# Performance work log

Measured on AMD Instinct MI355X. Metric: run time of the kernel, lower is better.

The kernel has to match this reference:

```python
import jax, jax.numpy as jnp
import numpy as np

NUM_HEADS = 16
ROPE_BASE = 2048.0


def _rope_tables(seq_len, head_dim, dtype):
    inv_freq = 1.0 / (ROPE_BASE ** (jnp.arange(0, head_dim, 2, dtype=jnp.float32) / head_dim))
    t = jnp.arange(seq_len, dtype=jnp.float32)
    freqs = jnp.einsum('i,j->ij', t, inv_freq)          # [N, D/2]
    emb = jnp.concatenate([freqs, freqs], axis=-1)       # [N, D]
    return jnp.cos(emb).astype(dtype), jnp.sin(emb).astype(dtype)


def _rotate_half(x):
    x1, x2 = jnp.split(x, 2, axis=-1)
    return jnp.concatenate([-x2, x1], axis=-1)


def setup_inputs() -> dict:
    key = jax.random.key(0)
    k1, k2, k3, k4 = jax.random.split(key, 4)
    B, N, C = 2, 2048, 1024
    x = jax.random.normal(k1, (B, N, C), dtype=jnp.float32)
    w_qkv = jax.random.normal(k2, (3 * C, C), dtype=jnp.float32) * (C ** -0.5)
    w_proj = jax.random.normal(k3, (C, C), dtype=jnp.float32) * (C ** -0.5)
    b_proj = jnp.zeros((C,), dtype=jnp.float32)
    key_padding_mask = jax.random.randint(k4, (B, N), 0, 2, dtype=jnp.int32)
    return {"x": x, "w_qkv": w_qkv, "w_proj": w_proj, "b_proj": b_proj,
            "key_padding_mask": key_padding_mask}


def reference(x, w_qkv, w_proj, b_proj, key_padding_mask):
    B, N, C = x.shape
    H = NUM_HEADS
    D = C // H
    scale = D ** -0.5

    qkv = x @ w_qkv.T                                    # [B, N, 3C]
    q, k, v = jnp.split(qkv, 3, axis=-1)
    # [B, N, C] -> [B, H, N, D]
    q = q.reshape(B, N, H, D).transpose(0, 2, 1, 3)
    k = k.reshape(B, N, H, D).transpose(0, 2, 1, 3)
    v = v.reshape(B, N, H, D).transpose(0, 2, 1, 3)

    cos, sin = _rope_tables(N, D, x.dtype)               # [N, D]
    q = q * cos + _rotate_half(q) * sin
    k = k * cos + _rotate_half(k) * sin

    attn = jnp.einsum('bhqd,bhkd->bhqk', q, k) * scale   # [B, H, N, N]
    mask = (key_padding_mask == 0)[:, None, None, :]     # [B, 1, 1, N]
    attn = jnp.where(mask, jnp.asarray(-1e9, attn.dtype), attn)
    attn = jax.nn.softmax(attn, axis=-1)

    out = jnp.einsum('bhqk,bhkd->bhqd', attn, v)         # [B, H, N, D]
    out = out.transpose(0, 2, 1, 3).reshape(B, N, C)
    return out @ w_proj.T + b_proj
```

## Files before the change

kernel.cpp:

```cpp
#include <hip/hip_runtime.h>


typedef __attribute__((ext_vector_type(8))) short          s16x8;
typedef __attribute__((ext_vector_type(8))) unsigned short u16x8;
typedef __attribute__((ext_vector_type(4))) unsigned short u16x4;
typedef __attribute__((ext_vector_type(4))) float          f32x4;

#define MFMA_BF16(a, b, c) __builtin_amdgcn_mfma_f32_16x16x32_bf16((a), (b), (c), 0, 0, 0)

#define GLD_TO_LDS(gp, lp) __builtin_amdgcn_global_load_lds(                  \
    (const __attribute__((address_space(1))) void*)(gp),                      \
    (__attribute__((address_space(3))) void*)(lp), 16, 0, 0)

__device__ __forceinline__ unsigned short f2bf(float f) {
    union { float f; unsigned int u; } v; v.f = f;
    unsigned int u = v.u;
    unsigned int r = u + 0x7FFFu + ((u >> 16) & 1u);
    return (unsigned short)(r >> 16);
}
__device__ __forceinline__ float bf2f(unsigned short h) {
    union { unsigned int u; float f; } v; v.u = ((unsigned int)h) << 16;
    return v.f;
}

__global__ __launch_bounds__(256) void prep(const float* __restrict__ x,
                                            const float* __restrict__ wqkv,
                                            const float* __restrict__ wproj,
                                            const int* __restrict__ m,
                                            unsigned short* __restrict__ xb,
                                            unsigned short* __restrict__ wqkvb,
                                            unsigned short* __restrict__ wprojb,
                                            unsigned short* __restrict__ mb) {
    int blk = blockIdx.x, tid = threadIdx.x;
    if (blk < 8192) {
        const float* src; unsigned short* dst; int i;
        if (blk < 4096)      { src = x;     dst = xb;     i = blk * 256 + tid; }
        else if (blk < 7168) { src = wqkv;  dst = wqkvb;  i = (blk - 4096) * 256 + tid; }
        else                 { src = wproj; dst = wprojb; i = (blk - 7168) * 256 + tid; }
        f32x4 v = ((const f32x4*)src)[i];
        u16x4 o;
        o[0] = f2bf(v[0]); o[1] = f2bf(v[1]); o[2] = f2bf(v[2]); o[3] = f2bf(v[3]);
        ((u16x4*)dst)[i] = o;
    } else {
        int i = (blk - 8192) * 256 + tid;
        mb[i] = (m[i] == 0) ? (unsigned short)0 : (unsigned short)0x3F80;
    }
}

__global__ __launch_bounds__(256) void gemm_bt(const unsigned short* __restrict__ A,
                                               const unsigned short* __restrict__ B,
                                               unsigned short* __restrict__ C,
                                               int M, int N, int K) {
    __shared__ unsigned short Al[128][64];
    __shared__ unsigned short Bl[128][64];
    const int tid  = threadIdx.x;
    const int lane = tid & 63;
    const int qd   = lane >> 4;
    const int cc   = lane & 15;
    const int wave = tid >> 6;
    const int wr   = wave >> 1, wc = wave & 1;
    const int m0   = blockIdx.y * 128, n0 = blockIdx.x * 128;
    unsigned short* Alf = &Al[0][0];
    unsigned short* Blf = &Bl[0][0];

    f32x4 acc[4][4];
#pragma unroll
    for (int i = 0; i < 4; i++)
#pragma unroll
        for (int j = 0; j < 4; j++) acc[i][j] = (f32x4){0.f, 0.f, 0.f, 0.f};

    for (int k0 = 0; k0 < K; k0 += 64) {
#pragma unroll
        for (int t = 0; t < 4; t++) {
            int idx = t * 256 + tid;
            int row = idx >> 3, sg = (idx & 7) ^ (row & 7);
            GLD_TO_LDS(A + (size_t)(m0 + row) * K + k0 + sg * 8, Alf + idx * 8);
            GLD_TO_LDS(B + (size_t)(n0 + row) * K + k0 + sg * 8, Blf + idx * 8);
        }
        __syncthreads();
#pragma unroll
        for (int ks = 0; ks < 64; ks += 32) {
            const int s4 = ks >> 3;
            s16x8 af[4], bf[4];
#pragma unroll
            for (int i = 0; i < 4; i++) {
                int r = wr * 64 + i * 16 + cc;
                af[i] = *(const s16x8*)&Al[r][((s4 + qd) ^ (r & 7)) * 8];
            }
#pragma unroll
            for (int j = 0; j < 4; j++) {
                int r = wc * 64 + j * 16 + cc;
                bf[j] = *(const s16x8*)&Bl[r][((s4 + qd) ^ (r & 7)) * 8];
            }
#pragma unroll
            for (int i = 0; i < 4; i++)
#pragma unroll
                for (int j = 0; j < 4; j++)
                    acc[i][j] = MFMA_BF16(af[i], bf[j], acc[i][j]);
        }
        __syncthreads();
    }
#pragma unroll
    for (int i = 0; i < 4; i++)
#pragma unroll
        for (int j = 0; j < 4; j++)
#pragma unroll
            for (int r = 0; r < 4; r++) {
                int row = m0 + wr * 64 + i * 16 + qd * 4 + r;
                int col = n0 + wc * 64 + j * 16 + cc;
                C[(size_t)row * N + col] = f2bf(acc[i][j][r]);
            }
}

__global__ __launch_bounds__(256) void rope_scatter(const unsigned short* __restrict__ qkv,
                                                    const int* __restrict__ msk,
                                                    unsigned short* __restrict__ Q,
                                                    unsigned short* __restrict__ Kg,
                                                    unsigned short* __restrict__ Vt) {
    const int N = 2048, H = 16, D = 64, C3 = 3072;
    const float SCL = 0.18033688f;
    __shared__ unsigned short vl[64][65];
    const int nt = blockIdx.x, h = blockIdx.y, b = blockIdx.z;
    const int n0 = nt * 64;
    const int tid = threadIdx.x;
    const size_t bh = (size_t)b * H + h;
#pragma unroll
    for (int it = 0; it < 2; it++) {
        int idx = tid + it * 256;
        int row = idx >> 3, seg = idx & 7;
        int d0 = seg * 8;
        int n = n0 + row;
        size_t rb = ((size_t)b * N + n) * C3;
        int keep = msk[(size_t)b * N + n];
        u16x8 qv = *(const u16x8*)&qkv[rb + h * 64 + d0];
        u16x8 qp = *(const u16x8*)&qkv[rb + h * 64 + (d0 ^ 32)];
        u16x8 kv = *(const u16x8*)&qkv[rb + 1024 + h * 64 + d0];
        u16x8 kp = *(const u16x8*)&qkv[rb + 1024 + h * 64 + (d0 ^ 32)];
        u16x8 vv = *(const u16x8*)&qkv[rb + 2048 + h * 64 + d0];
        u16x8 qo, ko;
        float sgn = (d0 < 32) ? -1.0f : 1.0f;
#pragma unroll
        for (int j = 0; j < 8; j++) {
            int jj = (d0 & 31) + j;
            float th = (float)n * exp2f(-0.34375f * (float)jj);
            float cth = cosf(th), sth = sinf(th);
            qo[j] = f2bf((bf2f(qv[j]) * cth + sgn * bf2f(qp[j]) * sth) * SCL);
            ko[j] = f2bf(bf2f(kv[j]) * cth + sgn * bf2f(kp[j]) * sth);
            vl[row][d0 + j] = keep ? vv[j] : (unsigned short)0;
        }
        *(u16x8*)&Q[(bh * N + n) * D + d0]  = qo;
        *(u16x8*)&Kg[(bh * N + n) * D + d0] = ko;
    }
    __syncthreads();
#pragma unroll
    for (int it = 0; it < 2; it++) {
        int idx = tid + it * 256;
        int drow = idx >> 3, nseg = idx & 7;
        u16x8 ov;
#pragma unroll
        for (int j = 0; j < 8; j++) ov[j] = vl[nseg * 8 + j][drow];
        *(u16x8*)&Vt[(bh * D + drow) * N + n0 + nseg * 8] = ov;
    }
}

__global__ __launch_bounds__(256, 2) void flash_attn(const unsigned short* __restrict__ Q,
                                                     const unsigned short* __restrict__ Kg,
                                                     const unsigned short* __restrict__ Vt,
                                                     const unsigned short* __restrict__ mb,
                                                     unsigned short* __restrict__ Og) {
    const int N = 2048, H = 16, D = 64;
    __shared__ unsigned short Kl0[64][64], Kl1[64][64];
    __shared__ unsigned short Vl0[64][64], Vl1[64][64];
    __shared__ unsigned short Pl[4][32][76];
    const int tid  = threadIdx.x;
    const int lane = tid & 63;
    const int wave = tid >> 6;
    const int qd   = lane >> 4;
    const int cc   = lane & 15;
    const int qt = blockIdx.x, h = blockIdx.y, b = blockIdx.z;
    const int q0 = qt * 128;
    const size_t bh = (size_t)b * H + h;

    s16x8 qf[2][2];
#pragma unroll
    for (int fr = 0; fr < 2; fr++) {
        const unsigned short* Qb = Q + (bh * N + q0 + wave * 32 + fr * 16 + cc) * D;
        qf[fr][0] = *(const s16x8*)(Qb + qd * 8);
        qf[fr][1] = *(const s16x8*)(Qb + 32 + qd * 8);
    }

    f32x4 o[2][4], lacc[2];
#pragma unroll
    for (int fr = 0; fr < 2; fr++) {
        lacc[fr] = (f32x4){0.f, 0.f, 0.f, 0.f};
#pragma unroll
        for (int db = 0; db < 4; db++) o[fr][db] = (f32x4){0.f, 0.f, 0.f, 0.f};
    }

    const unsigned short* Kbase = Kg + bh * N * D;
    const unsigned short* Vbase = Vt + bh * D * N;
    const unsigned short* mbase = mb + (size_t)b * N;
    const int row_s = tid >> 3, sg_s = (tid & 7) ^ ((tid >> 3) & 7);
    const int row_s2 = (tid + 256) >> 3, sg_s2 = (tid & 7) ^ (((tid + 256) >> 3) & 7);

    auto issue = [&](int k0, unsigned short* Kb, unsigned short* Vb) {
        GLD_TO_LDS(Kbase + (size_t)(k0 + row_s) * D + sg_s * 8,  Kb + tid * 8);
        GLD_TO_LDS(Vbase + (size_t)row_s * N + k0 + sg_s * 8,    Vb + tid * 8);
        GLD_TO_LDS(Kbase + (size_t)(k0 + row_s2) * D + sg_s2 * 8, Kb + (tid + 256) * 8);
        GLD_TO_LDS(Vbase + (size_t)row_s2 * N + k0 + sg_s2 * 8,   Vb + (tid + 256) * 8);
    };

    auto compute = [&](int k0, const unsigned short (*Kb)[64], const unsigned short (*Vb)[64]) {
        f32x4 sst[4][2];
        __builtin_amdgcn_s_setprio(1);
#pragma unroll
        for (int sub = 0; sub < 4; sub++) {
            int kr = sub * 16 + cc;
            s16x8 kf0 = *(const s16x8*)&Kb[kr][((0 + qd) ^ (kr & 7)) * 8];
            s16x8 kf1 = *(const s16x8*)&Kb[kr][((4 + qd) ^ (kr & 7)) * 8];
#pragma unroll
            for (int fr = 0; fr < 2; fr++) {
                f32x4 s = (f32x4){0.f, 0.f, 0.f, 0.f};
                s = MFMA_BF16(kf0, qf[fr][0], s);
                sst[sub][fr] = MFMA_BF16(kf1, qf[fr][1], s);
            }
        }
        __builtin_amdgcn_s_setprio(0);

        auto sm = [&](int sub) {
#pragma unroll
            for (int fr = 0; fr < 2; fr++) {
                f32x4 s = sst[sub][fr];
                float p0 = exp2f(s[0]);
                float p1 = exp2f(s[1]);
                float p2 = exp2f(s[2]);
                float p3 = exp2f(s[3]);
                unsigned int w0 = __builtin_amdgcn_perm(
                    __builtin_bit_cast(unsigned int, p1),
                    __builtin_bit_cast(unsigned int, p0), 0x07060302u);
                unsigned int w1 = __builtin_amdgcn_perm(
                    __builtin_bit_cast(unsigned int, p3),
                    __builtin_bit_cast(unsigned int, p2), 0x07060302u);
                unsigned long long w = ((unsigned long long)w1 << 32) | w0;
                *(unsigned long long*)&Pl[wave][fr * 16 + cc][sub * 16 + qd * 4] = w;
            }
        };

        auto pv = [&](int ks) {
            s16x8 mf = *(const s16x8*)&mbase[k0 + ks * 32 + qd * 8];
            s16x8 vfl[4];
#pragma unroll
            for (int db = 0; db < 4; db++) {
                int vr = db * 16 + cc;
                vfl[db] = *(const s16x8*)&Vb[vr][((ks * 4 + qd) ^ (vr & 7)) * 8];
            }
            __builtin_amdgcn_s_setprio(1);
#pragma unroll
            for (int fr = 0; fr < 2; fr++) {
                s16x8 pf = *(const s16x8*)&Pl[wave][fr * 16 + cc][ks * 32 + qd * 8];
                lacc[fr] = MFMA_BF16(pf, mf, lacc[fr]);
#pragma unroll
                for (int db = 0; db < 4; db++)
                    o[fr][db] = MFMA_BF16(pf, vfl[db], o[fr][db]);
            }
            __builtin_amdgcn_s_setprio(0);
        };

        sm(0); sm(1);
        pv(0);
        sm(2); sm(3);
        pv(1);
    };

    issue(0, &Kl0[0][0], &Vl0[0][0]);
    __syncthreads();
    for (int it = 0; it < 32; it += 2) {
        int k0 = it * 64;
        if (it + 1 < 32) issue(k0 + 64, &Kl1[0][0], &Vl1[0][0]);
        compute(k0, Kl0, Vl0);
        __syncthreads();
        if (it + 2 < 32) issue(k0 + 128, &Kl0[0][0], &Vl0[0][0]);
        compute(k0 + 64, Kl1, Vl1);
        __syncthreads();
    }

#pragma unroll
    for (int fr = 0; fr < 2; fr++) {
        float linv[4];
#pragma unroll
        for (int r = 0; r < 4; r++) linv[r] = 1.0f / lacc[fr][r];
#pragma unroll
        for (int db = 0; db < 4; db++)
#pragma unroll
            for (int r = 0; r < 4; r++) {
                int n = q0 + wave * 32 + fr * 16 + qd * 4 + r;
                Og[((size_t)b * N + n) * 1024 + h * 64 + db * 16 + cc] =
                    f2bf(o[fr][db][r] * linv[r]);
            }
    }
}

__global__ __launch_bounds__(256) void gemm_proj(const unsigned short* __restrict__ A,
                                                 const unsigned short* __restrict__ B,
                                                 float* __restrict__ C,
                                                 const float* __restrict__ bias) {
    const int NN = 1024, K = 1024;
    __shared__ unsigned short Al[128][64];
    __shared__ unsigned short Bl[64][64];
    const int tid  = threadIdx.x;
    const int lane = tid & 63;
    const int qd   = lane >> 4;
    const int cc   = lane & 15;
    const int wave = tid >> 6;
    const int wr   = wave >> 1, wc = wave & 1;
    const int m0   = blockIdx.y * 128, n0 = blockIdx.x * 64;
    unsigned short* Alf = &Al[0][0];
    unsigned short* Blf = &Bl[0][0];

    f32x4 acc[4][2];
#pragma unroll
    for (int i = 0; i < 4; i++)
#pragma unroll
        for (int j = 0; j < 2; j++) acc[i][j] = (f32x4){0.f, 0.f, 0.f, 0.f};

    for (int k0 = 0; k0 < K; k0 += 64) {
#pragma unroll
        for (int t = 0; t < 4; t++) {
            int idx = t * 256 + tid;
            int row = idx >> 3, sg = (idx & 7) ^ (row & 7);
            GLD_TO_LDS(A + (size_t)(m0 + row) * K + k0 + sg * 8, Alf + idx * 8);
        }
#pragma unroll
        for (int t = 0; t < 2; t++) {
            int idx = t * 256 + tid;
            int row = idx >> 3, sg = (idx & 7) ^ (row & 7);
            GLD_TO_LDS(B + (size_t)(n0 + row) * K + k0 + sg * 8, Blf + idx * 8);
        }
        __syncthreads();
#pragma unroll
        for (int ks = 0; ks < 64; ks += 32) {
            const int s4 = ks >> 3;
            s16x8 af[4], bf[2];
#pragma unroll
            for (int i = 0; i < 4; i++) {
                int r = wr * 64 + i * 16 + cc;
                af[i] = *(const s16x8*)&Al[r][((s4 + qd) ^ (r & 7)) * 8];
            }
#pragma unroll
            for (int j = 0; j < 2; j++) {
                int r = wc * 32 + j * 16 + cc;
                bf[j] = *(const s16x8*)&Bl[r][((s4 + qd) ^ (r & 7)) * 8];
            }
#pragma unroll
            for (int i = 0; i < 4; i++)
#pragma unroll
                for (int j = 0; j < 2; j++)
                    acc[i][j] = MFMA_BF16(af[i], bf[j], acc[i][j]);
        }
        __syncthreads();
    }
#pragma unroll
    for (int i = 0; i < 4; i++)
#pragma unroll
        for (int j = 0; j < 2; j++)
#pragma unroll
            for (int r = 0; r < 4; r++) {
                int row = m0 + wr * 64 + i * 16 + qd * 4 + r;
                int col = n0 + wc * 32 + j * 16 + cc;
                C[(size_t)row * NN + col] = acc[i][j][r] + bias[col];
            }
}

extern "C" void kernel_launch(void* const* d_in, const int* in_sizes, int n_in,
                              void* d_out, int out_size, void* d_ws, size_t ws_size,
                              hipStream_t stream) {
    const float* x      = (const float*)d_in[0];
    const float* w_qkv  = (const float*)d_in[1];
    const float* w_proj = (const float*)d_in[2];
    const float* b_proj = (const float*)d_in[3];
    const int*   mask   = (const int*)d_in[4];
    float* out = (float*)d_out;

    unsigned short* ws     = (unsigned short*)d_ws;
    unsigned short* xb     = ws;
    unsigned short* wqkvb  = xb     + (size_t)4096 * 1024;
    unsigned short* wprojb = wqkvb  + (size_t)3072 * 1024;
    unsigned short* qkv    = wprojb + (size_t)1024 * 1024;
    unsigned short* Qm     = qkv    + (size_t)4096 * 3072;
    unsigned short* Km     = Qm     + (size_t)32 * 2048 * 64;
    unsigned short* Vtm    = Km     + (size_t)32 * 2048 * 64;
    unsigned short* attno  = Vtm    + (size_t)32 * 2048 * 64;
    unsigned short* maskbf = attno  + (size_t)4096 * 1024;

    prep<<<8208, 256, 0, stream>>>(x, w_qkv, w_proj, mask, xb, wqkvb, wprojb, maskbf);
    gemm_bt<<<dim3(24, 32), 256, 0, stream>>>(xb, wqkvb, qkv, 4096, 3072, 1024);
    rope_scatter<<<dim3(32, 16, 2), 256, 0, stream>>>(qkv, mask, Qm, Km, Vtm);
    flash_attn<<<dim3(16, 16, 2), 256, 0, stream>>>(Qm, Km, Vtm, maskbf, attno);
    gemm_proj<<<dim3(16, 32), 256, 0, stream>>>(attno, wprojb, out, b_proj);
}
```

Before: 200.1 us.

## Split flash attention block into eight waves of sixteen query rows each

Doubles the flash attention block to 512 threads with each wave owning 16 query rows instead of 32. This halves per-wave accumulator registers and the per-thread K/V staging loads, aiming for more resident waves and better latency hiding. In exchange each K/V fragment read from LDS feeds only one query fragment, doubling LDS read traffic per MFMA. The mask fragment loads are hoisted to the start of each tile.

Result: no change. 199.4 us (-0.4%).

```diff
diff --git a/kernel.cpp b/kernel.cpp
--- a/kernel.cpp
+++ b/kernel.cpp
@@ -163,7 +163,7 @@
     }
 }
 
-__global__ __launch_bounds__(256, 2) void flash_attn(const unsigned short* __restrict__ Q,
+__global__ __launch_bounds__(512, 4) void flash_attn(const unsigned short* __restrict__ Q,
                                                      const unsigned short* __restrict__ Kg,
                                                      const unsigned short* __restrict__ Vt,
                                                      const unsigned short* __restrict__ mb,
@@ -171,7 +171,7 @@
     const int N = 2048, H = 16, D = 64;
     __shared__ unsigned short Kl0[64][64], Kl1[64][64];
     __shared__ unsigned short Vl0[64][64], Vl1[64][64];
-    __shared__ unsigned short Pl[4][32][76];
+    __shared__ unsigned short Pl[8][16][76];
     const int tid  = threadIdx.x;
     const int lane = tid & 63;
     const int wave = tid >> 6;
@@ -181,95 +181,80 @@
     const int q0 = qt * 128;
     const size_t bh = (size_t)b * H + h;
 
-    s16x8 qf[2][2];
-#pragma unroll
-    for (int fr = 0; fr < 2; fr++) {
-        const unsigned short* Qb = Q + (bh * N + q0 + wave * 32 + fr * 16 + cc) * D;
-        qf[fr][0] = *(const s16x8*)(Qb + qd * 8);
-        qf[fr][1] = *(const s16x8*)(Qb + 32 + qd * 8);
-    }
-
-    f32x4 o[2][4], lacc[2];
-#pragma unroll
-    for (int fr = 0; fr < 2; fr++) {
-        lacc[fr] = (f32x4){0.f, 0.f, 0.f, 0.f};
-#pragma unroll
-        for (int db = 0; db < 4; db++) o[fr][db] = (f32x4){0.f, 0.f, 0.f, 0.f};
-    }
+    s16x8 qf[2];
+    {
+        const unsigned short* Qb = Q + (bh * N + q0 + wave * 16 + cc) * D;
+        qf[0] = *(const s16x8*)(Qb + qd * 8);
+        qf[1] = *(const s16x8*)(Qb + 32 + qd * 8);
+    }
+
+    f32x4 o[4], lacc = (f32x4){0.f, 0.f, 0.f, 0.f};
+#pragma unroll
+    for (int db = 0; db < 4; db++) o[db] = (f32x4){0.f, 0.f, 0.f, 0.f};
 
     const unsigned short* Kbase = Kg + bh * N * D;
     const unsigned short* Vbase = Vt + bh * D * N;
     const unsigned short* mbase = mb + (size_t)b * N;
     const int row_s = tid >> 3, sg_s = (tid & 7) ^ ((tid >> 3) & 7);
-    const int row_s2 = (tid + 256) >> 3, sg_s2 = (tid & 7) ^ (((tid + 256) >> 3) & 7);
 
     auto issue = [&](int k0, unsigned short* Kb, unsigned short* Vb) {
-        GLD_TO_LDS(Kbase + (size_t)(k0 + row_s) * D + sg_s * 8,  Kb + tid * 8);
-        GLD_TO_LDS(Vbase + (size_t)row_s * N + k0 + sg_s * 8,    Vb + tid * 8);
-        GLD_TO_LDS(Kbase + (size_t)(k0 + row_s2) * D + sg_s2 * 8, Kb + (tid + 256) * 8);
-        GLD_TO_LDS(Vbase + (size_t)row_s2 * N + k0 + sg_s2 * 8,   Vb + (tid + 256) * 8);
+        GLD_TO_LDS(Kbase + (size_t)(k0 + row_s) * D + sg_s * 8, Kb + tid * 8);
+        GLD_TO_LDS(Vbase + (size_t)row_s * N + k0 + sg_s * 8,   Vb + tid * 8);
     };
 
     auto compute = [&](int k0, const unsigned short (*Kb)[64], const unsigned short (*Vb)[64]) {
-        f32x4 sst[4][2];
+        s16x8 mf0 = *(const s16x8*)&mbase[k0 + qd * 8];
+        s16x8 mf1 = *(const s16x8*)&mbase[k0 + 32 + qd * 8];
+
+        f32x4 sst[4];
         __builtin_amdgcn_s_setprio(1);
 #pragma unroll
         for (int sub = 0; sub < 4; sub++) {
             int kr = sub * 16 + cc;
             s16x8 kf0 = *(const s16x8*)&Kb[kr][((0 + qd) ^ (kr & 7)) * 8];
             s16x8 kf1 = *(const s16x8*)&Kb[kr][((4 + qd) ^ (kr & 7)) * 8];
-#pragma unroll
-            for (int fr = 0; fr < 2; fr++) {
-                f32x4 s = (f32x4){0.f, 0.f, 0.f, 0.f};
-                s = MFMA_BF16(kf0, qf[fr][0], s);
-                sst[sub][fr] = MFMA_BF16(kf1, qf[fr][1], s);
-            }
+            f32x4 s = (f32x4){0.f, 0.f, 0.f, 0.f};
+            s = MFMA_BF16(kf0, qf[0], s);
+            sst[sub] = MFMA_BF16(kf1, qf[1], s);
         }
         __builtin_amdgcn_s_setprio(0);
 
         auto sm = [&](int sub) {
-#pragma unroll
-            for (int fr = 0; fr < 2; fr++) {
-                f32x4 s = sst[sub][fr];
-                float p0 = exp2f(s[0]);
-                float p1 = exp2f(s[1]);
-                float p2 = exp2f(s[2]);
-                float p3 = exp2f(s[3]);
-                unsigned int w0 = __builtin_amdgcn_perm(
-                    __builtin_bit_cast(unsigned int, p1),
-                    __builtin_bit_cast(unsigned int, p0), 0x07060302u);
-                unsigned int w1 = __builtin_amdgcn_perm(
-                    __builtin_bit_cast(unsigned int, p3),
-                    __builtin_bit_cast(unsigned int, p2), 0x07060302u);
-                unsigned long long w = ((unsigned long long)w1 << 32) | w0;
-                *(unsigned long long*)&Pl[wave][fr * 16 + cc][sub * 16 + qd * 4] = w;
-            }
+            f32x4 s = sst[sub];
+            float p0 = exp2f(s[0]);
+            float p1 = exp2f(s[1]);
+            float p2 = exp2f(s[2]);
+            float p3 = exp2f(s[3]);
+            unsigned int w0 = __builtin_amdgcn_perm(
+                __builtin_bit_cast(unsigned int, p1),
+                __builtin_bit_cast(unsigned int, p0), 0x07060302u);
+            unsigned int w1 = __builtin_amdgcn_perm(
+                __builtin_bit_cast(unsigned int, p3),
+                __builtin_bit_cast(unsigned int, p2), 0x07060302u);
+            unsigned long long w = ((unsigned long long)w1 << 32) | w0;
+            *(unsigned long long*)&Pl[wave][cc][sub * 16 + qd * 4] = w;
         };
 
-        auto pv = [&](int ks) {
-            s16x8 mf = *(const s16x8*)&mbase[k0 + ks * 32 + qd * 8];
+        auto pv = [&](int ks, s16x8 mf) {
             s16x8 vfl[4];
 #pragma unroll
             for (int db = 0; db < 4; db++) {
                 int vr = db * 16 + cc;
                 vfl[db] = *(const s16x8*)&Vb[vr][((ks * 4 + qd) ^ (vr & 7)) * 8];
             }
+            s16x8 pf = *(const s16x8*)&Pl[wave][cc][ks * 32 + qd * 8];
             __builtin_amdgcn_s_setprio(1);
-#pragma unroll
-            for (int fr = 0; fr < 2; fr++) {
-                s16x8 pf = *(const s16x8*)&Pl[wave][fr * 16 + cc][ks * 32 + qd * 8];
-                lacc[fr] = MFMA_BF16(pf, mf, lacc[fr]);
-#pragma unroll
-                for (int db = 0; db < 4; db++)
-                    o[fr][db] = MFMA_BF16(pf, vfl[db], o[fr][db]);
-            }
+            lacc = MFMA_BF16(pf, mf, lacc);
+#pragma unroll
+            for (int db = 0; db < 4; db++)
+                o[db] = MFMA_BF16(pf, vfl[db], o[db]);
             __builtin_amdgcn_s_setprio(0);
         };
 
         sm(0); sm(1);
-        pv(0);
+        pv(0, mf0);
         sm(2); sm(3);
-        pv(1);
+        pv(1, mf1);
     };
 
     issue(0, &Kl0[0][0], &Vl0[0][0]);
@@ -284,20 +269,17 @@
         __syncthreads();
     }
 
-#pragma unroll
-    for (int fr = 0; fr < 2; fr++) {
-        float linv[4];
-#pragma unroll
-        for (int r = 0; r < 4; r++) linv[r] = 1.0f / lacc[fr][r];
-#pragma unroll
-        for (int db = 0; db < 4; db++)
-#pragma unroll
-            for (int r = 0; r < 4; r++) {
-                int n = q0 + wave * 32 + fr * 16 + qd * 4 + r;
-                Og[((size_t)b * N + n) * 1024 + h * 64 + db * 16 + cc] =
-                    f2bf(o[fr][db][r] * linv[r]);
-            }
-    }
+    float linv[4];
+#pragma unroll
+    for (int r = 0; r < 4; r++) linv[r] = 1.0f / lacc[r];
+#pragma unroll
+    for (int db = 0; db < 4; db++)
+#pragma unroll
+        for (int r = 0; r < 4; r++) {
+            int n = q0 + wave * 16 + qd * 4 + r;
+            Og[((size_t)b * N + n) * 1024 + h * 64 + db * 16 + cc] =
+                f2bf(o[db][r] * linv[r]);
+        }
 }
 
 __global__ __launch_bounds__(256) void gemm_proj(const unsigned short* __restrict__ A,
@@ -395,6 +377,6 @@
     prep<<<8208, 256, 0, stream>>>(x, w_qkv, w_proj, mask, xb, wqkvb, wprojb, maskbf);
     gemm_bt<<<dim3(24, 32), 256, 0, stream>>>(xb, wqkvb, qkv, 4096, 3072, 1024);
     rope_scatter<<<dim3(32, 16, 2), 256, 0, stream>>>(qkv, mask, Qm, Km, Vtm);
-    flash_attn<<<dim3(16, 16, 2), 256, 0, stream>>>(Qm, Km, Vtm, maskbf, attno);
+    flash_attn<<<dim3(16, 16, 2), 512, 0, stream>>>(Qm, Km, Vtm, maskbf, attno);
     gemm_proj<<<dim3(16, 32), 256, 0, stream>>>(attno, wprojb, out, b_proj);
 }
```

## Switch flash attention to 32x32 MFMA with register-resident P and permuted V/mask layout

Applied to the files above, without the earlier changes.

Moves the flash-attention kernel from 16x16x32 to 32x32x16 bf16 MFMAs. The QK^T output accumulator is fed straight into the PV MFMA as the A operand, which removes the per-wave LDS staging buffer for P. To make that register reuse valid, the prep and V-transpose kernels now permute key positions within each group of 16 so the mask and V^T columns line up with the 32x32 accumulator row ordering. This cuts LDS traffic and instruction count but relies on the permutation being exactly right and raises per-lane accumulator register use.

Measured after the change: 189.4 us. 1.06x faster.

```diff
diff --git a/kernel.cpp b/kernel.cpp
--- a/kernel.cpp
+++ b/kernel.cpp
@@ -5,8 +5,11 @@
 typedef __attribute__((ext_vector_type(8))) unsigned short u16x8;
 typedef __attribute__((ext_vector_type(4))) unsigned short u16x4;
 typedef __attribute__((ext_vector_type(4))) float          f32x4;
+typedef __attribute__((ext_vector_type(16))) float         f32x16;
+typedef __attribute__((ext_vector_type(4))) unsigned int   u32x4;
 
 #define MFMA_BF16(a, b, c) __builtin_amdgcn_mfma_f32_16x16x32_bf16((a), (b), (c), 0, 0, 0)
+#define MFMA32_BF16(a, b, c) __builtin_amdgcn_mfma_f32_32x32x16_bf16((a), (b), (c), 0, 0, 0)
 
 #define GLD_TO_LDS(gp, lp) __builtin_amdgcn_global_load_lds(                  \
     (const __attribute__((address_space(1))) void*)(gp),                      \
@@ -21,6 +24,19 @@
 __device__ __forceinline__ float bf2f(unsigned short h) {
     union { unsigned int u; float f; } v; v.u = ((unsigned int)h) << 16;
     return v.f;
+}
+__device__ __forceinline__ f32x16 zero16() {
+    f32x16 z;
+#pragma unroll
+    for (int i = 0; i < 16; i++) z[i] = 0.f;
+    return z;
+}
+__device__ __forceinline__ unsigned int pkbf(float a, float b) {
+    return __builtin_amdgcn_perm(__builtin_bit_cast(unsigned int, b),
+                                 __builtin_bit_cast(unsigned int, a), 0x07060302u);
+}
+__device__ __forceinline__ int perm16(int p) {
+    return (p & 3) + 8 * ((p >> 2) & 1) + 4 * (p >> 3);
 }
 
 __global__ __launch_bounds__(256) void prep(const float* __restrict__ x,
@@ -43,7 +59,8 @@
         ((u16x4*)dst)[i] = o;
     } else {
         int i = (blk - 8192) * 256 + tid;
-        mb[i] = (m[i] == 0) ? (unsigned short)0 : (unsigned short)0x3F80;
+        int src = (i & ~15) | perm16(i & 15);
+        mb[i] = (m[src] == 0) ? (unsigned short)0 : (unsigned short)0x3F80;
     }
 }
 
@@ -158,7 +175,11 @@
         int drow = idx >> 3, nseg = idx & 7;
         u16x8 ov;
 #pragma unroll
-        for (int j = 0; j < 8; j++) ov[j] = vl[nseg * 8 + j][drow];
+        for (int j = 0; j < 8; j++) {
+            int cpos = nseg * 8 + j;
+            int srcl = (cpos & ~15) | perm16(cpos & 15);
+            ov[j] = vl[srcl][drow];
+        }
         *(u16x8*)&Vt[(bh * D + drow) * N + n0 + nseg * 8] = ov;
     }
 }
@@ -171,31 +192,24 @@
     const int N = 2048, H = 16, D = 64;
     __shared__ unsigned short Kl0[64][64], Kl1[64][64];
     __shared__ unsigned short Vl0[64][64], Vl1[64][64];
-    __shared__ unsigned short Pl[4][32][76];
     const int tid  = threadIdx.x;
     const int lane = tid & 63;
     const int wave = tid >> 6;
-    const int qd   = lane >> 4;
-    const int cc   = lane & 15;
+    const int c    = lane & 31;
+    const int hi   = lane >> 5;
     const int qt = blockIdx.x, h = blockIdx.y, b = blockIdx.z;
     const int q0 = qt * 128;
     const size_t bh = (size_t)b * H + h;
 
-    s16x8 qf[2][2];
-#pragma unroll
-    for (int fr = 0; fr < 2; fr++) {
-        const unsigned short* Qb = Q + (bh * N + q0 + wave * 32 + fr * 16 + cc) * D;
-        qf[fr][0] = *(const s16x8*)(Qb + qd * 8);
-        qf[fr][1] = *(const s16x8*)(Qb + 32 + qd * 8);
-    }
-
-    f32x4 o[2][4], lacc[2];
-#pragma unroll
-    for (int fr = 0; fr < 2; fr++) {
-        lacc[fr] = (f32x4){0.f, 0.f, 0.f, 0.f};
-#pragma unroll
-        for (int db = 0; db < 4; db++) o[fr][db] = (f32x4){0.f, 0.f, 0.f, 0.f};
-    }
+    s16x8 qf[4];
+    {
+        const unsigned short* Qb = Q + (bh * N + q0 + wave * 32 + c) * D;
+#pragma unroll
+        for (int kd = 0; kd < 4; kd++) qf[kd] = *(const s16x8*)(Qb + kd * 16 + hi * 8);
+    }
+
+    f32x16 o[2], lacc;
+    o[0] = zero16(); o[1] = zero16(); lacc = zero16();
 
     const unsigned short* Kbase = Kg + bh * N * D;
     const unsigned short* Vbase = Vt + bh * D * N;
@@ -204,72 +218,61 @@
     const int row_s2 = (tid + 256) >> 3, sg_s2 = (tid & 7) ^ (((tid + 256) >> 3) & 7);
 
     auto issue = [&](int k0, unsigned short* Kb, unsigned short* Vb) {
-        GLD_TO_LDS(Kbase + (size_t)(k0 + row_s) * D + sg_s * 8,  Kb + tid * 8);
-        GLD_TO_LDS(Vbase + (size_t)row_s * N + k0 + sg_s * 8,    Vb + tid * 8);
+        GLD_TO_LDS(Kbase + (size_t)(k0 + row_s) * D + sg_s * 8,   Kb + tid * 8);
+        GLD_TO_LDS(Vbase + (size_t)row_s * N + k0 + sg_s * 8,     Vb + tid * 8);
         GLD_TO_LDS(Kbase + (size_t)(k0 + row_s2) * D + sg_s2 * 8, Kb + (tid + 256) * 8);
         GLD_TO_LDS(Vbase + (size_t)row_s2 * N + k0 + sg_s2 * 8,   Vb + (tid + 256) * 8);
     };
 
     auto compute = [&](int k0, const unsigned short (*Kb)[64], const unsigned short (*Vb)[64]) {
-        f32x4 sst[4][2];
+        f32x16 sst[2];
         __builtin_amdgcn_s_setprio(1);
 #pragma unroll
-        for (int sub = 0; sub < 4; sub++) {
-            int kr = sub * 16 + cc;
-            s16x8 kf0 = *(const s16x8*)&Kb[kr][((0 + qd) ^ (kr & 7)) * 8];
-            s16x8 kf1 = *(const s16x8*)&Kb[kr][((4 + qd) ^ (kr & 7)) * 8];
-#pragma unroll
-            for (int fr = 0; fr < 2; fr++) {
-                f32x4 s = (f32x4){0.f, 0.f, 0.f, 0.f};
-                s = MFMA_BF16(kf0, qf[fr][0], s);
-                sst[sub][fr] = MFMA_BF16(kf1, qf[fr][1], s);
-            }
+        for (int kg = 0; kg < 2; kg++) {
+            int kr = kg * 32 + c;
+            f32x16 s = zero16();
+#pragma unroll
+            for (int kd = 0; kd < 4; kd++) {
+                s16x8 kf = *(const s16x8*)&Kb[kr][((kd * 2 + hi) ^ (kr & 7)) * 8];
+                s = MFMA32_BF16(kf, qf[kd], s);
+            }
+            sst[kg] = s;
         }
         __builtin_amdgcn_s_setprio(0);
 
-        auto sm = [&](int sub) {
-#pragma unroll
-            for (int fr = 0; fr < 2; fr++) {
-                f32x4 s = sst[sub][fr];
-                float p0 = exp2f(s[0]);
-                float p1 = exp2f(s[1]);
-                float p2 = exp2f(s[2]);
-                float p3 = exp2f(s[3]);
-                unsigned int w0 = __builtin_amdgcn_perm(
-                    __builtin_bit_cast(unsigned int, p1),
-                    __builtin_bit_cast(unsigned int, p0), 0x07060302u);
-                unsigned int w1 = __builtin_amdgcn_perm(
-                    __builtin_bit_cast(unsigned int, p3),
-                    __builtin_bit_cast(unsigned int, p2), 0x07060302u);
-                unsigned long long w = ((unsigned long long)w1 << 32) | w0;
-                *(unsigned long long*)&Pl[wave][fr * 16 + cc][sub * 16 + qd * 4] = w;
+        auto packkg = [&](int kg, s16x8* pa) {
+            float p[16];
+#pragma unroll
+            for (int r = 0; r < 16; r++) p[r] = __builtin_amdgcn_exp2f(sst[kg][r]);
+#pragma unroll
+            for (int half = 0; half < 2; half++) {
+                int bs = half * 8;
+                u32x4 w = { pkbf(p[bs + 0], p[bs + 1]), pkbf(p[bs + 2], p[bs + 3]),
+                            pkbf(p[bs + 4], p[bs + 5]), pkbf(p[bs + 6], p[bs + 7]) };
+                pa[half] = __builtin_bit_cast(s16x8, w);
             }
         };
 
-        auto pv = [&](int ks) {
-            s16x8 mf = *(const s16x8*)&mbase[k0 + ks * 32 + qd * 8];
-            s16x8 vfl[4];
-#pragma unroll
-            for (int db = 0; db < 4; db++) {
-                int vr = db * 16 + cc;
-                vfl[db] = *(const s16x8*)&Vb[vr][((ks * 4 + qd) ^ (vr & 7)) * 8];
-            }
+        auto pvks = [&](int ks, s16x8 pf) {
+            s16x8 mfr = *(const s16x8*)&mbase[k0 + ks * 16 + hi * 8];
             __builtin_amdgcn_s_setprio(1);
-#pragma unroll
-            for (int fr = 0; fr < 2; fr++) {
-                s16x8 pf = *(const s16x8*)&Pl[wave][fr * 16 + cc][ks * 32 + qd * 8];
-                lacc[fr] = MFMA_BF16(pf, mf, lacc[fr]);
-#pragma unroll
-                for (int db = 0; db < 4; db++)
-                    o[fr][db] = MFMA_BF16(pf, vfl[db], o[fr][db]);
+            lacc = MFMA32_BF16(pf, mfr, lacc);
+#pragma unroll
+            for (int db = 0; db < 2; db++) {
+                int vr = db * 32 + c;
+                s16x8 vf = *(const s16x8*)&Vb[vr][((ks * 2 + hi) ^ (vr & 7)) * 8];
+                o[db] = MFMA32_BF16(pf, vf, o[db]);
             }
             __builtin_amdgcn_s_setprio(0);
         };
 
-        sm(0); sm(1);
-        pv(0);
-        sm(2); sm(3);
-        pv(1);
+        s16x8 pa[2];
+        packkg(0, pa);
+        pvks(0, pa[0]);
+        pvks(1, pa[1]);
+        packkg(1, pa);
+        pvks(2, pa[0]);
+        pvks(3, pa[1]);
     };
 
     issue(0, &Kl0[0][0], &Vl0[0][0]);
@@ -284,20 +287,17 @@
         __syncthreads();
     }
 
-#pragma unroll
-    for (int fr = 0; fr < 2; fr++) {
-        float linv[4];
-#pragma unroll
-        for (int r = 0; r < 4; r++) linv[r] = 1.0f / lacc[fr][r];
-#pragma unroll
-        for (int db = 0; db < 4; db++)
-#pragma unroll
-            for (int r = 0; r < 4; r++) {
-                int n = q0 + wave * 32 + fr * 16 + qd * 4 + r;
-                Og[((size_t)b * N + n) * 1024 + h * 64 + db * 16 + cc] =
-                    f2bf(o[fr][db][r] * linv[r]);
-            }
-    }
+    float linv[16];
+#pragma unroll
+    for (int r = 0; r < 16; r++) linv[r] = 1.0f / lacc[r];
+#pragma unroll
+    for (int db = 0; db < 2; db++)
+#pragma unroll
+        for (int r = 0; r < 16; r++) {
+            int n = q0 + wave * 32 + (r & 3) + 8 * (r >> 2) + 4 * hi;
+            Og[((size_t)b * N + n) * 1024 + h * 64 + db * 32 + c] =
+                f2bf(o[db][r] * linv[r]);
+        }
 }
 
 __global__ __launch_bounds__(256) void gemm_proj(const unsigned short* __restrict__ A,
```
